# Kernel optimization log

Hardware: AMD Instinct MI355X
Metric: run time of the kernel (lower is better)

Reference implementation:

```python
import jax, jax.numpy as jnp
import numpy as np

IN_CH = 256
OUT_CH = 64
HEADS = 8


def setup_inputs() -> dict:
    key = jax.random.key(0)
    ks = jax.random.split(key, 7)
    N = 4096
    proj = OUT_CH * HEADS
    s_in = 1.0 / np.sqrt(IN_CH)
    return {
        "query_input": jax.random.normal(ks[0], (N, IN_CH), dtype=jnp.float32),
        "Wq": jax.random.uniform(ks[1], (proj, IN_CH), jnp.float32, -s_in, s_in),
        "bq": jax.random.uniform(ks[2], (proj,), jnp.float32, -s_in, s_in),
        "Wk": jax.random.uniform(ks[3], (proj, IN_CH), jnp.float32, -s_in, s_in),
        "bk": jax.random.uniform(ks[4], (proj,), jnp.float32, -s_in, s_in),
        "Wv": jax.random.uniform(ks[5], (proj, IN_CH), jnp.float32, -s_in, s_in),
        "bv": jax.random.uniform(ks[6], (proj,), jnp.float32, -s_in, s_in),
    }


def reference(query_input, Wq, bq, Wk, bk, Wv, bv):
    N = query_input.shape[0]
    # projections -> [N, H, M]
    q = (query_input @ Wq.T + bq).reshape(N, HEADS, OUT_CH)
    k = (query_input @ Wk.T + bk).reshape(N, HEADS, OUT_CH)
    v = (query_input @ Wv.T + bv).reshape(N, HEADS, OUT_CH)
    # sigmoid attention scores [N, L, H]
    attention_num = jax.nn.sigmoid(jnp.einsum('nhm,lhm->nlh', q, k))
    # sum-normalization over L (keys)
    normalizer = attention_num.sum(axis=1, keepdims=True)  # [N, 1, H]
    attention = attention_num / normalizer
    # weighted V reduction [N, H, D], then mean over heads -> [N, D]
    out = jnp.einsum('nlh,lhd->nhd', attention, v).mean(axis=1)
    return out
```

## Files before the change

### kernel.cpp

```cpp
#include <hip/hip_runtime.h>
#include <hip/hip_bf16.h>
#include <math.h>

#define N_TOK 4096
#define IN_CH 256
#define OUT_CH 64
#define HEADS 8
#define PROJ (OUT_CH * HEADS)
#define NLOG2E -1.44269504088896340736f

typedef float f32x4 __attribute__((ext_vector_type(4)));
typedef __bf16 bf16x8 __attribute__((ext_vector_type(8)));
typedef unsigned short ushort_t;

__device__ inline ushort_t bf16rne(float x) {
    unsigned u = __float_as_uint(x);
    unsigned r = (u + 0x7FFFu + ((u >> 16) & 1u)) >> 16;
    return (ushort_t)r;
}

__global__ __launch_bounds__(256) void cast_pack_kernel(
    const float* __restrict__ X,
    const float* __restrict__ Wq, const float* __restrict__ Wk,
    const float* __restrict__ Wv,
    ushort_t* __restrict__ Xa, ushort_t* __restrict__ Wp)
{
    const int i = blockIdx.x * 256 + threadIdx.x;
    const float* src;
    ushort_t* dst;
    float scale = 1.0f;
    if (i < 131072) {
        const int t = i & 15, quad = (i >> 4) & 3, k8 = (i >> 6) & 7, g = i >> 9;
        src = X + (size_t)(g * 16 + t) * IN_CH + k8 * 32 + quad * 8;
        dst = Xa + (size_t)i * 8;
    } else {
        const int j = i - 131072;
        const int z = j >> 14;
        const int r = j & 16383;
        const int cl = r & 15, quad = (r >> 4) & 3, k8 = (r >> 6) & 7, gc = r >> 9;
        const float* W = (z == 0) ? Wq : (z == 1) ? Wk : Wv;
        src = W + (size_t)(gc * 16 + cl) * IN_CH + k8 * 32 + quad * 8;
        dst = Wp + (size_t)z * 131072 * 8 + (size_t)r * 8;
        if (z == 0) scale = NLOG2E;
    }
    float4 a = *(const float4*)src;
    float4 b = *(const float4*)(src + 4);
    ushort_t pk[8];
    pk[0] = bf16rne(a.x * scale); pk[1] = bf16rne(a.y * scale);
    pk[2] = bf16rne(a.z * scale); pk[3] = bf16rne(a.w * scale);
    pk[4] = bf16rne(b.x * scale); pk[5] = bf16rne(b.y * scale);
    pk[6] = bf16rne(b.z * scale); pk[7] = bf16rne(b.w * scale);
    *(uint4*)dst = *(uint4*)pk;
}

__global__ __launch_bounds__(256) void proj_mfma_kernel(
    const ushort_t* __restrict__ Xa, const ushort_t* __restrict__ Wp,
    const float* __restrict__ bq, const float* __restrict__ bk,
    const float* __restrict__ bv,
    ushort_t* __restrict__ Qb, ushort_t* __restrict__ Kb,
    ushort_t* __restrict__ Vt)
{
    const int z = blockIdx.z;
    const float* bias = (z == 0) ? bq : (z == 1) ? bk : bv;
    const float bscale = (z == 0) ? NLOG2E : 1.0f;
    const int c0 = blockIdx.x * 64;
    const int n0 = blockIdx.y * 64;

    const int tid = threadIdx.x;
    const int w = tid >> 6;
    const int lane = tid & 63;
    const int l15 = lane & 15;
    const int quad = lane >> 4;

    const ushort_t* xa = Xa + (size_t)(blockIdx.y * 4 + w) * 4096 + quad * 128 + l15 * 8;
    const ushort_t* wp0 = Wp + (size_t)z * 131072 * 8 +
                          (size_t)(blockIdx.x * 4) * 4096 + quad * 128 + l15 * 8;

    f32x4 acc[4] = {{0.f, 0.f, 0.f, 0.f}, {0.f, 0.f, 0.f, 0.f},
                    {0.f, 0.f, 0.f, 0.f}, {0.f, 0.f, 0.f, 0.f}};

#pragma unroll
    for (int k8 = 0; k8 < 8; ++k8) {
        bf16x8 a = *(const bf16x8*)(xa + k8 * 512);
#pragma unroll
        for (int f = 0; f < 4; ++f) {
            bf16x8 b = *(const bf16x8*)(wp0 + f * 4096 + k8 * 512);
            acc[f] = __builtin_amdgcn_mfma_f32_16x16x32_bf16(a, b, acc[f], 0, 0, 0);
        }
    }

    if (z < 2) {
        ushort_t* out = z ? Kb : Qb;
#pragma unroll
        for (int f = 0; f < 4; ++f) {
            const float bb = bias[c0 + f * 16 + l15] * bscale;
#pragma unroll
            for (int r = 0; r < 4; ++r) {
                const int tok = n0 + w * 16 + quad * 4 + r;
                out[(size_t)tok * PROJ + c0 + f * 16 + l15] = bf16rne(acc[f][r] + bb);
            }
        }
    } else {
#pragma unroll
        for (int f = 0; f < 4; ++f) {
            const int c = c0 + f * 16 + l15;
            const float bb = bias[c];
            ushort4 pk;
            pk.x = bf16rne(acc[f][0] + bb);
            pk.y = bf16rne(acc[f][1] + bb);
            pk.z = bf16rne(acc[f][2] + bb);
            pk.w = bf16rne(acc[f][3] + bb);
            *(ushort4*)&Vt[(size_t)c * N_TOK + n0 + w * 16 + quad * 4] = pk;
        }
    }
}

__global__ __launch_bounds__(256, 4) void attn_kernel(
    const ushort_t* __restrict__ Qb, const ushort_t* __restrict__ Kb,
    const ushort_t* __restrict__ Vt,
    float* __restrict__ NUM, float* __restrict__ DEN)
{
    const int h = blockIdx.y;
    const int z = blockIdx.z;
    const int n0 = blockIdx.x * 64;
    const int tid = threadIdx.x;
    const int w = tid >> 6;
    const int lane = tid & 63;
    const int l15 = lane & 15;
    const int quad = lane >> 4;

    __shared__ ushort_t Ks[64 * 64];
    __shared__ ushort_t Vs[64 * 64];
    __shared__ ushort_t Ps[4][16 * 72];

    bf16x8 qb[2];
    {
        const ushort_t* base = Qb + (size_t)(n0 + w * 16 + l15) * PROJ + h * 64 + quad * 8;
        qb[0] = *(const bf16x8*)(base);
        qb[1] = *(const bf16x8*)(base + 32);
    }

    bf16x8 onesv;
#pragma unroll
    for (int j = 0; j < 8; ++j) onesv[j] = (__bf16)1.0f;

    f32x4 o[4] = {{0.f, 0.f, 0.f, 0.f}, {0.f, 0.f, 0.f, 0.f},
                  {0.f, 0.f, 0.f, 0.f}, {0.f, 0.f, 0.f, 0.f}};
    f32x4 dacc = {0.f, 0.f, 0.f, 0.f};

    const int srow = tid >> 2;
    const int sc2 = (tid & 3) * 2;
    const int sp0 = (sc2 ^ (srow & 7)) * 8;
    const int sp1 = ((sc2 + 1) ^ (srow & 7)) * 8;
    const int xm = l15 & 7;
    const int rofA = (quad ^ xm) * 8;
    const int rofB = ((4 + quad) ^ xm) * 8;

    const ushort_t* kgbase = Kb + (size_t)h * 64 + sc2 * 8;
    const ushort_t* vgbase = Vt + (size_t)h * 64 * N_TOK + (size_t)srow * N_TOK + sc2 * 8;

    for (int lt = 0; lt < 32; ++lt) {
        const int l0 = z * 2048 + lt * 64;
        __syncthreads();
        {
            const uint4* kg = (const uint4*)(kgbase + (size_t)(l0 + srow) * PROJ);
            uint4 k0 = kg[0], k1 = kg[1];
            const uint4* vg = (const uint4*)(vgbase + l0);
            uint4 v0 = vg[0], v1 = vg[1];
            *(uint4*)&Ks[srow * 64 + sp0] = k0;
            *(uint4*)&Ks[srow * 64 + sp1] = k1;
            *(uint4*)&Vs[srow * 64 + sp0] = v0;
            *(uint4*)&Vs[srow * 64 + sp1] = v1;
        }
        __syncthreads();

        f32x4 s[4] = {{0.f, 0.f, 0.f, 0.f}, {0.f, 0.f, 0.f, 0.f},
                      {0.f, 0.f, 0.f, 0.f}, {0.f, 0.f, 0.f, 0.f}};
#pragma unroll
        for (int f = 0; f < 4; ++f) {
            bf16x8 ka = *(const bf16x8*)&Ks[(f * 16 + l15) * 64 + rofA];
            s[f] = __builtin_amdgcn_mfma_f32_16x16x32_bf16(ka, qb[0], s[f], 0, 0, 0);
        }
#pragma unroll
        for (int f = 0; f < 4; ++f) {
            bf16x8 ka = *(const bf16x8*)&Ks[(f * 16 + l15) * 64 + rofB];
            s[f] = __builtin_amdgcn_mfma_f32_16x16x32_bf16(ka, qb[1], s[f], 0, 0, 0);
        }

        ushort_t* pw = &Ps[w][l15 * 72];
#pragma unroll
        for (int f = 0; f < 4; ++f) {
            float p0 = __builtin_amdgcn_rcpf(1.0f + __builtin_amdgcn_exp2f(s[f][0]));
            float p1 = __builtin_amdgcn_rcpf(1.0f + __builtin_amdgcn_exp2f(s[f][1]));
            float p2 = __builtin_amdgcn_rcpf(1.0f + __builtin_amdgcn_exp2f(s[f][2]));
            float p3 = __builtin_amdgcn_rcpf(1.0f + __builtin_amdgcn_exp2f(s[f][3]));
            unsigned u0 = __float_as_uint(p0) + 0x8000u;
            unsigned u1 = __float_as_uint(p1) + 0x8000u;
            unsigned u2 = __float_as_uint(p2) + 0x8000u;
            unsigned u3 = __float_as_uint(p3) + 0x8000u;
            uint2 pk;
            pk.x = __builtin_amdgcn_perm(u1, u0, 0x07060302u);
            pk.y = __builtin_amdgcn_perm(u3, u2, 0x07060302u);
            *(uint2*)&pw[f * 16 + quad * 4] = pk;
        }

#pragma unroll
        for (int c = 0; c < 2; ++c) {
            bf16x8 pa = *(const bf16x8*)&Ps[w][l15 * 72 + c * 32 + quad * 8];
            const int rof = c ? rofB : rofA;
#pragma unroll
            for (int f = 0; f < 4; ++f) {
                bf16x8 vb = *(const bf16x8*)&Vs[(f * 16 + l15) * 64 + rof];
                o[f] = __builtin_amdgcn_mfma_f32_16x16x32_bf16(pa, vb, o[f], 0, 0, 0);
            }
            dacc = __builtin_amdgcn_mfma_f32_16x16x32_bf16(pa, onesv, dacc, 0, 0, 0);
        }
    }

#pragma unroll
    for (int f = 0; f < 4; ++f) {
#pragma unroll
        for (int r = 0; r < 4; ++r) {
            const int q = n0 + w * 16 + quad * 4 + r;
            NUM[((size_t)z * N_TOK + q) * PROJ + h * 64 + f * 16 + l15] = o[f][r];
        }
    }
    if (l15 == 0) {
#pragma unroll
        for (int r = 0; r < 4; ++r)
            DEN[((size_t)z * N_TOK + n0 + w * 16 + quad * 4 + r) * HEADS + h] = dacc[r];
    }
}

__global__ __launch_bounds__(256) void reduce_kernel(
    const float* __restrict__ NUM, const float* __restrict__ DEN,
    float* __restrict__ out)
{
    const int g = blockIdx.x * 256 + threadIdx.x;
    const int n = g >> 6;
    const int d = g & 63;
    float acc = 0.0f;
#pragma unroll
    for (int hh = 0; hh < HEADS; ++hh) {
        float num = NUM[(size_t)n * PROJ + hh * 64 + d] +
                    NUM[((size_t)N_TOK + n) * PROJ + hh * 64 + d];
        float dd = DEN[(size_t)n * HEADS + hh] +
                   DEN[((size_t)N_TOK + n) * HEADS + hh];
        acc += num / dd;
    }
    out[g] = acc * 0.125f;
}

extern "C" void kernel_launch(void* const* d_in, const int* in_sizes, int n_in,
                              void* d_out, int out_size, void* d_ws, size_t ws_size,
                              hipStream_t stream) {
    (void)in_sizes; (void)n_in; (void)out_size; (void)ws_size;
    const float* X  = (const float*)d_in[0];
    const float* Wq = (const float*)d_in[1];
    const float* bq = (const float*)d_in[2];
    const float* Wk = (const float*)d_in[3];
    const float* bk = (const float*)d_in[4];
    const float* Wv = (const float*)d_in[5];
    const float* bv = (const float*)d_in[6];
    float* out = (float*)d_out;

    float* NUM = (float*)d_ws;
    float* DEN = NUM + (size_t)2 * N_TOK * PROJ;
    ushort_t* Qb = (ushort_t*)(DEN + (size_t)2 * N_TOK * HEADS);
    ushort_t* Kb = Qb + (size_t)N_TOK * PROJ;
    ushort_t* Vt = Kb + (size_t)N_TOK * PROJ;
    ushort_t* Xa = Vt + (size_t)N_TOK * PROJ;
    ushort_t* Wp = Xa + (size_t)N_TOK * IN_CH;

    cast_pack_kernel<<<dim3(704), 256, 0, stream>>>(X, Wq, Wk, Wv, Xa, Wp);
    proj_mfma_kernel<<<dim3(PROJ / 64, N_TOK / 64, 3), 256, 0, stream>>>(
        Xa, Wp, bq, bk, bv, Qb, Kb, Vt);
    attn_kernel<<<dim3(N_TOK / 64, HEADS, 2), 256, 0, stream>>>(
        Qb, Kb, Vt, NUM, DEN);
    reduce_kernel<<<dim3(N_TOK * OUT_CH / 256), 256, 0, stream>>>(NUM, DEN, out);
}
```

Baseline: 144.1 us.

## Stage projection epilogue through LDS and prefetch next K/V tile into registers

The projection kernel now writes its bias-added bf16 tile into shared memory, then each thread emits coalesced 16-byte stores for Q/K rows and for the transposed V, replacing scattered 2-byte and 8-byte global stores. Its k-loop unroll is reduced to 2. The attention kernel loads the next K/V tile into registers while the current tile is being computed, hiding global load latency behind the MFMA and sigmoid work. The trade-off is extra LDS and a barrier in the projection kernel, plus higher register pressure in the attention kernel, which could lower occupancy.

```diff
diff --git a/kernel.cpp b/kernel.cpp
--- a/kernel.cpp
+++ b/kernel.cpp
@@ -72,6 +72,8 @@
     const int l15 = lane & 15;
     const int quad = lane >> 4;
 
+    __shared__ ushort_t Es[64 * 68];
+
     const ushort_t* xa = Xa + (size_t)(blockIdx.y * 4 + w) * 4096 + quad * 128 + l15 * 8;
     const ushort_t* wp0 = Wp + (size_t)z * 131072 * 8 +
                           (size_t)(blockIdx.x * 4) * 4096 + quad * 128 + l15 * 8;
@@ -79,7 +81,7 @@
     f32x4 acc[4] = {{0.f, 0.f, 0.f, 0.f}, {0.f, 0.f, 0.f, 0.f},
                     {0.f, 0.f, 0.f, 0.f}, {0.f, 0.f, 0.f, 0.f}};
 
-#pragma unroll
+#pragma unroll 2
     for (int k8 = 0; k8 < 8; ++k8) {
         bf16x8 a = *(const bf16x8*)(xa + k8 * 512);
 #pragma unroll
@@ -90,28 +92,37 @@
     }
 
     if (z < 2) {
+#pragma unroll
+        for (int f = 0; f < 4; ++f) {
+            const float bb = bias[c0 + f * 16 + l15] * bscale;
+#pragma unroll
+            for (int r = 0; r < 4; ++r)
+                Es[(w * 16 + quad * 4 + r) * 68 + f * 16 + l15] = bf16rne(acc[f][r] + bb);
+        }
+    } else {
+#pragma unroll
+        for (int f = 0; f < 4; ++f) {
+            const float bb = bias[c0 + f * 16 + l15];
+#pragma unroll
+            for (int r = 0; r < 4; ++r)
+                Es[(f * 16 + l15) * 68 + w * 16 + quad * 4 + r] = bf16rne(acc[f][r] + bb);
+        }
+    }
+    __syncthreads();
+
+    const int erow = tid >> 2;
+    const int ecol = (tid & 3) * 16;
+    uint4 pk0 = *(uint4*)&Es[erow * 68 + ecol];
+    uint4 pk1 = *(uint4*)&Es[erow * 68 + ecol + 8];
+    if (z < 2) {
         ushort_t* out = z ? Kb : Qb;
-#pragma unroll
-        for (int f = 0; f < 4; ++f) {
-            const float bb = bias[c0 + f * 16 + l15] * bscale;
-#pragma unroll
-            for (int r = 0; r < 4; ++r) {
-                const int tok = n0 + w * 16 + quad * 4 + r;
-                out[(size_t)tok * PROJ + c0 + f * 16 + l15] = bf16rne(acc[f][r] + bb);
-            }
-        }
+        ushort_t* p = &out[(size_t)(n0 + erow) * PROJ + c0 + ecol];
+        *(uint4*)p = pk0;
+        *(uint4*)(p + 8) = pk1;
     } else {
-#pragma unroll
-        for (int f = 0; f < 4; ++f) {
-            const int c = c0 + f * 16 + l15;
-            const float bb = bias[c];
-            ushort4 pk;
-            pk.x = bf16rne(acc[f][0] + bb);
-            pk.y = bf16rne(acc[f][1] + bb);
-            pk.z = bf16rne(acc[f][2] + bb);
-            pk.w = bf16rne(acc[f][3] + bb);
-            *(ushort4*)&Vt[(size_t)c * N_TOK + n0 + w * 16 + quad * 4] = pk;
-        }
+        ushort_t* p = &Vt[(size_t)(c0 + erow) * N_TOK + n0 + ecol];
+        *(uint4*)p = pk0;
+        *(uint4*)(p + 8) = pk1;
     }
 }
 
@@ -156,23 +167,28 @@
     const int rofA = (quad ^ xm) * 8;
     const int rofB = ((4 + quad) ^ xm) * 8;
 
-    const ushort_t* kgbase = Kb + (size_t)h * 64 + sc2 * 8;
-    const ushort_t* vgbase = Vt + (size_t)h * 64 * N_TOK + (size_t)srow * N_TOK + sc2 * 8;
+    const ushort_t* kgp = Kb + (size_t)h * 64 + sc2 * 8 +
+                          (size_t)(z * 2048 + srow) * PROJ;
+    const ushort_t* vgp = Vt + (size_t)h * 64 * N_TOK + (size_t)srow * N_TOK +
+                          sc2 * 8 + z * 2048;
+
+    uint4 kr0 = ((const uint4*)kgp)[0], kr1 = ((const uint4*)kgp)[1];
+    uint4 vr0 = ((const uint4*)vgp)[0], vr1 = ((const uint4*)vgp)[1];
 
     for (int lt = 0; lt < 32; ++lt) {
-        const int l0 = z * 2048 + lt * 64;
         __syncthreads();
-        {
-            const uint4* kg = (const uint4*)(kgbase + (size_t)(l0 + srow) * PROJ);
-            uint4 k0 = kg[0], k1 = kg[1];
-            const uint4* vg = (const uint4*)(vgbase + l0);
-            uint4 v0 = vg[0], v1 = vg[1];
-            *(uint4*)&Ks[srow * 64 + sp0] = k0;
-            *(uint4*)&Ks[srow * 64 + sp1] = k1;
-            *(uint4*)&Vs[srow * 64 + sp0] = v0;
-            *(uint4*)&Vs[srow * 64 + sp1] = v1;
-        }
+        *(uint4*)&Ks[srow * 64 + sp0] = kr0;
+        *(uint4*)&Ks[srow * 64 + sp1] = kr1;
+        *(uint4*)&Vs[srow * 64 + sp0] = vr0;
+        *(uint4*)&Vs[srow * 64 + sp1] = vr1;
         __syncthreads();
+
+        if (lt < 31) {
+            kgp += 64 * PROJ;
+            vgp += 64;
+            kr0 = ((const uint4*)kgp)[0]; kr1 = ((const uint4*)kgp)[1];
+            vr0 = ((const uint4*)vgp)[0]; vr1 = ((const uint4*)vgp)[1];
+        }
 
         f32x4 s[4] = {{0.f, 0.f, 0.f, 0.f}, {0.f, 0.f, 0.f, 0.f},
                       {0.f, 0.f, 0.f, 0.f}, {0.f, 0.f, 0.f, 0.f}};
```

After: 143.2 us. No clear change (-0.6%).
